# Optimization experiments

Hardware: AMD Instinct MI355X
Metric: run time of the kernel (lower is better)

The kernel has to match this reference:

```python
import jax, jax.numpy as jnp
import numpy as np
import math

DIM = 1024      # dim == dim_attn (required by value-reshape)
HEAD = 16
KV = 128        # K_v routing slots
HD = DIM // HEAD
N = 50000       # number of nodes


def setup_inputs() -> dict:
    key = jax.random.key(0)
    ks = jax.random.split(key, 8)
    s = lambda fan_in: 1.0 / np.sqrt(fan_in)
    return {
        "x": jax.random.normal(ks[0], (N, DIM), jnp.float32),
        "node_index": jax.random.normal(ks[1], (N, 4), jnp.float32),
        # nn.Linear(dim, dim_attn)
        "Wq": jax.random.normal(ks[2], (DIM, DIM), jnp.float32) * s(DIM),
        "bq": jnp.zeros((DIM,), jnp.float32),
        # nn.Parameter key (K_v, head, head_dim), torch.randn init
        "key_p": jax.random.normal(ks[3], (KV, HEAD, HD), jnp.float32),
        # nn.Linear(dim, dim)
        "Wv": jax.random.normal(ks[4], (DIM, DIM), jnp.float32) * s(DIM),
        "bv": jnp.zeros((DIM,), jnp.float32),
        # gate params, shape (head, 1)
        "alpha": jnp.full((HEAD, 1), math.log(9.0), jnp.float32),
        "beta": jnp.full((HEAD, 1), math.log(0.01), jnp.float32),
        # nn.Linear(4, head*K_v)
        "Wb": jax.random.normal(ks[5], (HEAD * KV, 4), jnp.float32) * s(4),
        "bb": jnp.zeros((HEAD * KV,), jnp.float32),
    }


def _mh_sinkhorn(A, num_iters=3, eps=0.05):
    # A: (N, H, K). Faithful to the per-head torch sinkhorn (Q transposed to
    # (K, N)): row sums are over the node axis, col sums over the slot axis.
    n = A.shape[0]
    k = A.shape[2]
    Q = jnp.exp(A / eps)
    Q = Q / jnp.sum(Q, axis=(0, 2), keepdims=True)          # total-sum norm per head
    for _ in range(num_iters):
        Q = Q / jnp.sum(Q, axis=0, keepdims=True) / k       # rows of Q.T (per slot)
        Q = Q / jnp.sum(Q, axis=2, keepdims=True) / n       # cols of Q.T (per node)
    return Q * n


def reference(x, node_index, Wq, bq, key_p, Wv, bv, alpha, beta, Wb, bb):
    n = x.shape[0]
    q = (x @ Wq.T + bq).reshape(n, HEAD, HD)
    attn = jnp.einsum('nhd,rhd->nhr', q, key_p) / np.float32(np.sqrt(HD))
    bias = (node_index @ Wb.T + bb).reshape(n, HEAD, KV)
    attn = attn + bias                                       # (n, H, K_v)
    xv = (x @ Wv.T + bv).reshape(n, HEAD, HD)
    v = jnp.einsum('nhr,nhd->rhd', jax.nn.sigmoid(attn), xv)  # (K_v, H, D)
    cons = _mh_sinkhorn(jax.nn.softmax(attn, axis=-1))
    v = jnp.einsum('nhr,rhd->nhd', cons, v)
    out = jax.nn.sigmoid(alpha) * xv + jax.nn.sigmoid(beta) * v  # (H,1) broadcasts
    return out.reshape(n, DIM)
```

## Files before the change

kernel.cpp:

```cpp
#include <hip/hip_runtime.h>

#define N_NODES 50000
#define MPAD    50176
#define DIM     1024
#define HEAD    16
#define KV      128
#define HD      64
#define NGRP    98

typedef unsigned short ushort_t;
typedef short short8 __attribute__((ext_vector_type(8)));
typedef float f32x4 __attribute__((ext_vector_type(4)));

__device__ inline unsigned short f2bf(float f){
  union { float f; unsigned u; } v; v.f = f;
  unsigned u = v.u;
  unsigned r = (u + 0x7FFFu + ((u >> 16) & 1u)) >> 16;
  return (unsigned short)r;
}
__device__ inline float bf2f(unsigned short u){
  union { unsigned u; float f; } v; v.u = ((unsigned)u) << 16; return v.f;
}

__device__ inline void gload_lds16(const void* g, void* l){
  __builtin_amdgcn_global_load_lds(
      (const __attribute__((address_space(1))) void*)g,
      (__attribute__((address_space(3))) void*)l, 16, 0, 0);
}

__device__ inline short8 frag64(const ushort_t* lds, int row, int kk, int lane){
  int c  = kk*4 + (lane >> 4);
  int cc = c ^ (row & 7);
  return *(const short8*)(lds + row*64 + cc*8);
}
__device__ inline short8 frag128(const ushort_t* lds, int row, int kk, int lane){
  int c  = kk*4 + (lane >> 4);
  int cc = c ^ (row & 7);
  return *(const short8*)(lds + row*128 + cc*8);
}
__device__ inline short8 frag32(const ushort_t* lds, int row, int lane){
  int p = (lane >> 4) ^ ((row >> 1) & 3);
  return *(const short8*)(lds + row*32 + p*8);
}

__global__ void k_zero(float* p, int n){
  int i = blockIdx.x*256 + threadIdx.x;
  if (i < n) p[i] = 0.f;
}

__global__ void k_prep_x(const float* __restrict__ x, ushort_t* __restrict__ x_bf){
  int idx = blockIdx.x*256 + threadIdx.x;
  int row = idx >> 7, c = idx & 127;
  const float4* s = (const float4*)(x + (size_t)row*1024 + c*8);
  float4 f0 = s[0], f1 = s[1];
  short8 v;
  v[0]=(short)f2bf(f0.x); v[1]=(short)f2bf(f0.y); v[2]=(short)f2bf(f0.z); v[3]=(short)f2bf(f0.w);
  v[4]=(short)f2bf(f1.x); v[5]=(short)f2bf(f1.y); v[6]=(short)f2bf(f1.z); v[7]=(short)f2bf(f1.w);
  int sc = (c & ~3) | ((c ^ (row >> 1)) & 3);
  *(short8*)(x_bf + (size_t)row*1024 + sc*8) = v;
}

__global__ void k_prep_w(const float* __restrict__ Wq, const float* __restrict__ Wv,
                         ushort_t* __restrict__ w_bf){
  int idx = blockIdx.x*256 + threadIdx.x;
  int j = idx >> 10, k = idx & 1023;
  float v = (j < 1024) ? Wq[idx] : Wv[(size_t)(j-1024)*1024 + k];
  int l = k >> 3;
  int q = (l & ~3) | ((l ^ (j >> 1)) & 3);
  w_bf[(size_t)j*1024 + q*8 + (k & 7)] = f2bf(v);
}

__global__ void k_prep_key(const float* __restrict__ key_p, ushort_t* __restrict__ key_bf){
  int idx = blockIdx.x*256 + threadIdx.x;
  int h = idx >> 13, rem = idx & 8191;
  int r = rem >> 6, d = rem & 63;
  float v = key_p[(size_t)(r*HEAD + h)*HD + d];
  int pos = ((((d>>3) ^ (r & 7)) & 7) << 3) | (d & 7);
  key_bf[(size_t)h*8192 + r*64 + pos] = f2bf(v);
}

__global__ void k_vreduce(const float* __restrict__ vp, float* __restrict__ vout){
  int i = blockIdx.x*256 + threadIdx.x;
  float s = 0.f;
  for (int gg = 0; gg < NGRP; ++gg) s += vp[(size_t)gg*131072 + i];
  vout[i] = s;
}

__global__ __launch_bounds__(512) void k_gemm(const ushort_t* __restrict__ x_bf,
    const ushort_t* __restrict__ w_bf, const float* __restrict__ bq,
    const float* __restrict__ bv, ushort_t* __restrict__ q_bf, float* xv_out){
  extern __shared__ char gsm[];
  ushort_t* As = (ushort_t*)gsm;
  ushort_t* Bs = (ushort_t*)(gsm + 65536);
  const int tid = threadIdx.x, lane = tid & 63;
  const int wid = tid >> 6, wr = wid >> 2, wc = wid & 3;
  int b = blockIdx.x;
  int wg = (b & 7)*196 + (b >> 3);
  const int bm0 = (wg >> 3) * 256, bn0 = (wg & 7) * 256;

  f32x4 acc[8][4];
  #pragma unroll
  for (int m=0;m<8;m++)
    #pragma unroll
    for (int n=0;n<4;n++) acc[m][n] = (f32x4){0.f,0.f,0.f,0.f};

  const ushort_t* asrc = x_bf + (size_t)bm0*1024;
  const ushort_t* bsrc = w_bf + (size_t)bn0*1024;

#define STAGE(kt, si)                                                     \
  { _Pragma("unroll")                                                     \
    for (int it=0; it<2; ++it){                                           \
      int chunk = it*512 + tid;                                           \
      int r = chunk >> 2, c = chunk & 3;                                  \
      gload_lds16(asrc + (size_t)r*1024 + (kt)*32 + c*8,                  \
                  As + (si)*8192 + chunk*8);                              \
      gload_lds16(bsrc + (size_t)r*1024 + (kt)*32 + c*8,                  \
                  Bs + (si)*8192 + chunk*8);                              \
    }                                                                     \
  }

  STAGE(0, 0);
  STAGE(1, 1);
  STAGE(2, 2);

  for (int t = 0; t < 32; ++t){
    const int cur = t & 3;
    if (t < 30)      { asm volatile("s_waitcnt vmcnt(8)" ::: "memory"); }
    else if (t < 31) { asm volatile("s_waitcnt vmcnt(4)" ::: "memory"); }
    else             { asm volatile("s_waitcnt vmcnt(0)" ::: "memory"); }
    __builtin_amdgcn_s_barrier();
    __builtin_amdgcn_sched_barrier(0);
    if (t + 3 < 32) STAGE(t+3, (t+3)&3);

    const ushort_t* ab  = As + cur*8192;
    const ushort_t* bb_ = Bs + cur*8192;
    short8 bfr[4];
    #pragma unroll
    for (int n=0;n<4;n++) bfr[n] = frag32(bb_, wc*64 + n*16 + (lane&15), lane);
    #pragma unroll
    for (int m=0;m<8;m++){
      short8 af = frag32(ab, wr*128 + m*16 + (lane&15), lane);
      #pragma unroll
      for (int n=0;n<4;n++)
        acc[m][n] = __builtin_amdgcn_mfma_f32_16x16x32_bf16(af, bfr[n], acc[m][n], 0,0,0);
    }
    __builtin_amdgcn_s_barrier();
  }
#undef STAGE

  __syncthreads();

  const bool isq = bn0 < 1024;
  float biasv[4];
  #pragma unroll
  for (int n=0;n<4;n++){
    int col = bn0 + wc*64 + n*16 + (lane & 15);
    biasv[n] = isq ? bq[col] : bv[col - 1024];
  }

  if (isq){
    ushort_t* img = (ushort_t*)gsm;
    #pragma unroll
    for (int n=0;n<4;n++){
      int lcol = wc*64 + n*16 + (lane & 15);
      int d = lcol & 63;
      #pragma unroll
      for (int m=0;m<8;m++){
        #pragma unroll
        for (int j=0;j<4;j++){
          int lrow = wr*128 + m*16 + (lane>>4)*4 + j;
          int sc = (lcol & ~63) | ((((d>>3) ^ (lrow & 7)) & 7) << 3) | (d & 7);
          img[lrow*256 + sc] = f2bf(acc[m][n][j] + biasv[n]);
        }
      }
    }
    __syncthreads();
    #pragma unroll
    for (int it=0; it<16; ++it){
      int r  = it*16 + (tid >> 5);
      int ch = tid & 31;
      short8 v = *(const short8*)(img + r*256 + ch*8);
      *(short8*)(q_bf + (size_t)(bm0 + r)*1024 + bn0 + ch*8) = v;
    }
  } else {
    #pragma unroll
    for (int n=0;n<4;n++){
      int col = bn0 + wc*64 + n*16 + (lane & 15);
      #pragma unroll
      for (int m=0;m<8;m++){
        #pragma unroll
        for (int j=0;j<4;j++){
          int row = bm0 + wr*128 + m*16 + (lane>>4)*4 + j;
          if (row < N_NODES)
            xv_out[(size_t)row*1024 + (col - 1024)] = acc[m][n][j] + biasv[n];
        }
      }
    }
  }
}

template<int PHASE>
__global__ __launch_bounds__(256) void k_attn(
    const ushort_t* __restrict__ q_bf, const ushort_t* __restrict__ key_bf,
    const float* __restrict__ node_index, const float* __restrict__ Wb,
    const float* __restrict__ bb, const float* __restrict__ colsum_in,
    float* __restrict__ colsum_out, const float* __restrict__ v_fin,
    float* __restrict__ v_part, float* xv_out,
    const float* __restrict__ alpha, const float* __restrict__ beta)
{
  constexpr int QB    = (PHASE == 2) ? 1 : 2;
  constexpr int O_Q   = 0;
  constexpr int O_KEY = O_Q + QB*8192;
  constexpr int O_NI  = O_KEY + 16384;
  constexpr int O_WB  = O_NI + QB*1024;
  constexpr int O_RED = O_WB + 2560;
  constexpr int O_COL = O_RED + 2048;
  constexpr int O_W   = O_COL + 512;
  constexpr int O_X1  = O_W + 512;
  constexpr int O_X2  = O_X1 + 16384;

  extern __shared__ char smem[];
  ushort_t* q_lds   = (ushort_t*)(smem + O_Q);
  ushort_t* key_lds = (ushort_t*)(smem + O_KEY);
  float* ni_lds  = (float*)(smem + O_NI);
  float* wb_lds  = (float*)(smem + O_WB);
  float* red_lds = (float*)(smem + O_RED);
  float* col_acc = (float*)(smem + O_COL);
  float* w_lds   = (float*)(smem + O_W);
  ushort_t* sigT     = (ushort_t*)(smem + O_X1);
  ushort_t* xvT      = (ushort_t*)(smem + O_X2);
  ushort_t* vT       = (ushort_t*)(smem + O_X1);
  ushort_t* cons_lds = (ushort_t*)(smem + O_X2);
  float*    out_lds  = (float*)(smem + O_X2);

  const int tid = threadIdx.x, lane = tid & 63, wid = tid >> 6;
  const int h    = blockIdx.x & 15;
  const int g    = blockIdx.x >> 4;
  const int base = g * 512;
  int NT = (MPAD - base) >> 6; if (NT > 8) NT = 8;

  #pragma unroll
  for (int it = 0; it < 4; ++it){
    int chunk = it*256 + tid;
    gload_lds16(key_bf + (size_t)h*8192 + chunk*8, key_lds + chunk*8);
  }
  #pragma unroll
  for (int it = 0; it < 2; ++it){
    int chunk = it*256 + tid;
    int r = chunk >> 3, c = chunk & 7;
    gload_lds16(q_bf + (size_t)(base + r)*1024 + h*64 + c*8, q_lds + chunk*8);
  }
  { int r = tid >> 2, c = tid & 3;
    ni_lds[tid] = (base + r < N_NODES) ? node_index[(size_t)(base + r)*4 + c] : 0.f; }
  if (tid < 128){
    #pragma unroll
    for (int c=0;c<4;c++) wb_lds[tid*5+c] = Wb[(size_t)(h*128 + tid)*4 + c];
    wb_lds[tid*5+4] = bb[h*128 + tid];
    if (PHASE >= 1) w_lds[tid] = 1.f / (128.f * colsum_in[h*128 + tid]);
    if (PHASE <= 1) col_acc[tid] = 0.f;
  }
  if constexpr (PHASE == 2){
    int r = tid >> 1, dh = (tid & 1)*32;
    #pragma unroll
    for (int i=0;i<32;i++){
      int d = dh + i;
      vT[d*128 + ((r>>3) ^ (d&7))*8 + (r&7)] = f2bf(v_fin[((size_t)r*16 + h)*64 + d]);
    }
  }
  float xvr[16], xvn[16];
  if constexpr (PHASE == 0){
    int d = tid & 63, q4 = tid >> 6;
    #pragma unroll
    for (int i=0;i<16;i++){
      int row = base + q4*16 + i;
      xvr[i] = (row < N_NODES) ? xv_out[(size_t)row*1024 + h*64 + d] : 0.f;
    }
  }
  f32x4 vac[2][4];
  if constexpr (PHASE == 0)
    for (int m=0;m<2;m++) for (int n=0;n<4;n++) vac[m][n] = (f32x4){0.f,0.f,0.f,0.f};

  __syncthreads();

  for (int t = 0; t < NT; ++t){
    const int i0  = base + t*64;
    const int cur = t & 1;
    const ushort_t* qb  = q_lds  + ((QB==2) ? cur*4096 : 0);
    const float*    nib = ni_lds + ((QB==2) ? cur*256  : 0);
    float ni_next = 0.f;

    if constexpr (QB == 2){
      if (t+1 < NT){
        int i1 = i0 + 64;
        #pragma unroll
        for (int it = 0; it < 2; ++it){
          int chunk = it*256 + tid;
          int r = chunk >> 3, c = chunk & 7;
          gload_lds16(q_bf + (size_t)(i1 + r)*1024 + h*64 + c*8,
                      q_lds + (cur^1)*4096 + chunk*8);
        }
        int r = tid >> 2, c = tid & 3;
        ni_next = (i0 + 64 + r < N_NODES) ? node_index[(size_t)(i0+64+r)*4 + c] : 0.f;
      }
    } else {
      if (t+1 < NT){
        int r = tid >> 2, c = tid & 3;
        ni_next = (i0 + 64 + r < N_NODES) ? node_index[(size_t)(i0+64+r)*4 + c] : 0.f;
      }
    }
    if constexpr (PHASE == 0){
      if (t+1 < NT){
        int d = tid & 63, q4 = tid >> 6;
        #pragma unroll
        for (int i=0;i<16;i++){
          int row = i0 + 64 + q4*16 + i;
          xvn[i] = (row < N_NODES) ? xv_out[(size_t)row*1024 + h*64 + d] : 0.f;
        }
      }
    }

    f32x4 acc[2][4];
    for (int m=0;m<2;m++) for (int n=0;n<4;n++) acc[m][n] = (f32x4){0.f,0.f,0.f,0.f};
    #pragma unroll
    for (int kk = 0; kk < 2; ++kk){
      short8 kf[2];
      #pragma unroll
      for (int m=0;m<2;m++) kf[m] = frag64(key_lds, wid*32 + m*16 + (lane&15), kk, lane);
      #pragma unroll
      for (int n=0;n<4;n++){
        short8 qf = frag64(qb, n*16 + (lane&15), kk, lane);
        #pragma unroll
        for (int m=0;m<2;m++)
          acc[m][n] = __builtin_amdgcn_mfma_f32_16x16x32_bf16(kf[m], qf, acc[m][n], 0,0,0);
      }
    }

    float nif[4][4];
    #pragma unroll
    for (int n=0;n<4;n++){
      int nn = n*16 + (lane&15);
      #pragma unroll
      for (int c=0;c<4;c++) nif[n][c] = nib[nn*4+c];
    }
    float a[2][4][4];
    #pragma unroll
    for (int m=0;m<2;m++){
      #pragma unroll
      for (int j=0;j<4;j++){
        int r = wid*32 + m*16 + (lane>>4)*4 + j;
        float w0 = wb_lds[r*5+0], w1 = wb_lds[r*5+1];
        float w2 = wb_lds[r*5+2], w3 = wb_lds[r*5+3], w4 = wb_lds[r*5+4];
        #pragma unroll
        for (int n=0;n<4;n++){
          float b = w4 + w0*nif[n][0] + w1*nif[n][1] + w2*nif[n][2] + w3*nif[n][3];
          a[m][n][j] = acc[m][n][j]*0.125f + b;
        }
      }
    }

    float vmask[4];
    #pragma unroll
    for (int n=0;n<4;n++) vmask[n] = (i0 + n*16 + (lane&15) < N_NODES) ? 1.f : 0.f;

    if constexpr (PHASE == 0){
      #pragma unroll
      for (int m=0;m<2;m++) for (int n=0;n<4;n++) for (int j=0;j<4;j++){
        int r  = wid*32 + m*16 + (lane>>4)*4 + j;
        int nn = n*16 + (lane&15);
        float sg = vmask[n] / (1.f + __expf(-a[m][n][j]));
        sigT[r*64 + ((((nn>>3) ^ (r&7)) & 7) << 3) + (nn&7)] = f2bf(sg);
      }
      { int d = tid & 63, q4 = tid >> 6;
        #pragma unroll
        for (int i=0;i<16;i++){
          int nn = q4*16 + i;
          xvT[d*64 + ((((nn>>3) ^ (d&7)) & 7) << 3) + (nn&7)] = f2bf(xvr[i]);
        }
      }
    }

    float pm[4];
    #pragma unroll
    for (int n=0;n<4;n++){
      float m0 = a[0][n][0];
      #pragma unroll
      for (int m=0;m<2;m++) for (int j=0;j<4;j++) m0 = fmaxf(m0, a[m][n][j]);
      m0 = fmaxf(m0, __shfl_xor(m0, 16));
      m0 = fmaxf(m0, __shfl_xor(m0, 32));
      pm[n] = m0;
    }
    if (lane < 16){
      #pragma unroll
      for (int n=0;n<4;n++) red_lds[wid*64 + n*16 + lane] = pm[n];
    }
    __syncthreads();

    if constexpr (QB == 1){
      if (t+1 < NT){
        int i1 = i0 + 64;
        #pragma unroll
        for (int it = 0; it < 2; ++it){
          int chunk = it*256 + tid;
          int r = chunk >> 3, c = chunk & 7;
          gload_lds16(q_bf + (size_t)(i1 + r)*1024 + h*64 + c*8, q_lds + chunk*8);
        }
        ni_lds[tid] = ni_next;
      }
    }

    float mnn[4], snn[4];
    #pragma unroll
    for (int n=0;n<4;n++){
      int nn = n*16 + (lane&15);
      float m0 = red_lds[nn];
      m0 = fmaxf(m0, red_lds[64+nn]); m0 = fmaxf(m0, red_lds[128+nn]); m0 = fmaxf(m0, red_lds[192+nn]);
      mnn[n] = m0;
    }
    #pragma unroll
    for (int n=0;n<4;n++){
      float s = 0.f;
      #pragma unroll
      for (int m=0;m<2;m++) for (int j=0;j<4;j++){
        float e = __expf(a[m][n][j] - mnn[n]);
        a[m][n][j] = e; s += e;
      }
      s += __shfl_xor(s, 16); s += __shfl_xor(s, 32);
      snn[n] = s;
    }
    if (lane < 16){
      #pragma unroll
      for (int n=0;n<4;n++) red_lds[256 + wid*64 + n*16 + lane] = snn[n];
    }

    if constexpr (PHASE == 0){
      #pragma unroll
      for (int kk=0;kk<2;kk++){
        short8 sa[2];
        #pragma unroll
        for (int m=0;m<2;m++) sa[m] = frag64(sigT, wid*32 + m*16 + (lane&15), kk, lane);
        #pragma unroll
        for (int n=0;n<4;n++){
          short8 xf = frag64(xvT, n*16 + (lane&15), kk, lane);
          #pragma unroll
          for (int m=0;m<2;m++)
            vac[m][n] = __builtin_amdgcn_mfma_f32_16x16x32_bf16(sa[m], xf, vac[m][n], 0,0,0);
        }
      }
    }
    __syncthreads();

    #pragma unroll
    for (int n=0;n<4;n++){
      int nn = n*16 + (lane&15);
      snn[n] = red_lds[256+nn] + red_lds[256+64+nn] + red_lds[256+128+nn] + red_lds[256+192+nn];
    }
    #pragma unroll
    for (int n=0;n<4;n++){
      float inv = 20.f / snn[n];
      #pragma unroll
      for (int m=0;m<2;m++) for (int j=0;j<4;j++)
        a[m][n][j] = __expf(a[m][n][j] * inv);
    }

    float uval[4];
    if constexpr (PHASE >= 1){
      #pragma unroll
      for (int n=0;n<4;n++){
        float s = 0.f;
        #pragma unroll
        for (int m=0;m<2;m++){
          #pragma unroll
          for (int j=0;j<4;j++){
            int r = wid*32 + m*16 + (lane>>4)*4 + j;
            s += a[m][n][j] * w_lds[r];
          }
        }
        s += __shfl_xor(s, 16); s += __shfl_xor(s, 32);
        uval[n] = s;
      }
      if (lane < 16){
        #pragma unroll
        for (int n=0;n<4;n++) red_lds[wid*64 + n*16 + lane] = uval[n];
      }
      __syncthreads();
      #pragma unroll
      for (int n=0;n<4;n++){
        int nn = n*16 + (lane&15);
        float s = red_lds[nn] + red_lds[64+nn] + red_lds[128+nn] + red_lds[192+nn];
        uval[n] = 1.f / (50000.f * s);
      }
    }

    if constexpr (PHASE <= 1){
      float cs[2][4];
      #pragma unroll
      for (int m=0;m<2;m++){
        #pragma unroll
        for (int j=0;j<4;j++){
          float s = 0.f;
          #pragma unroll
          for (int n=0;n<4;n++){
            float tv = a[m][n][j] * vmask[n];
            if (PHASE == 1) tv *= uval[n];
            s += tv;
          }
          s += __shfl_xor(s, 1); s += __shfl_xor(s, 2);
          s += __shfl_xor(s, 4); s += __shfl_xor(s, 8);
          cs[m][j] = s;
        }
      }
      if ((lane & 15) == 0){
        #pragma unroll
        for (int m=0;m<2;m++) for (int j=0;j<4;j++){
          int r = wid*32 + m*16 + (lane>>4)*4 + j;
          col_acc[r] += cs[m][j];
        }
      }
    }

    if constexpr (PHASE == 2){
      #pragma unroll
      for (int m=0;m<2;m++) for (int n=0;n<4;n++) for (int j=0;j<4;j++){
        int r  = wid*32 + m*16 + (lane>>4)*4 + j;
        int nn = n*16 + (lane&15);
        float cv = 50000.f * uval[n] * a[m][n][j] * w_lds[r];
        cons_lds[nn*128 + ((r>>3) ^ (nn&7))*8 + (r&7)] = f2bf(cv);
      }
      __syncthreads();
      f32x4 oac[4];
      for (int n=0;n<4;n++) oac[n] = (f32x4){0.f,0.f,0.f,0.f};
      #pragma unroll
      for (int kk=0;kk<4;kk++){
        short8 va = frag128(vT, wid*16 + (lane&15), kk, lane);
        #pragma unroll
        for (int n=0;n<4;n++){
          short8 cf = frag128(cons_lds, n*16 + (lane&15), kk, lane);
          oac[n] = __builtin_amdgcn_mfma_f32_16x16x32_bf16(va, cf, oac[n], 0,0,0);
        }
      }
      __syncthreads();
      #pragma unroll
      for (int n=0;n<4;n++) for (int j=0;j<4;j++){
        int d  = wid*16 + (lane>>4)*4 + j;
        int nn = n*16 + (lane&15);
        out_lds[nn*68 + d] = oac[n][j];
      }
      __syncthreads();
      float sa = 1.f/(1.f + __expf(-alpha[h]));
      float sb = 1.f/(1.f + __expf(-beta[h]));
      int nn = tid >> 2, d0 = (tid & 3)*16;
      if (i0 + nn < N_NODES){
        #pragma unroll
        for (int gq=0; gq<4; ++gq){
          float4 vf = *(const float4*)(out_lds + nn*68 + d0 + gq*4);
          float4 xf = *(const float4*)(xv_out + (size_t)(i0+nn)*1024 + h*64 + d0 + gq*4);
          float4 o;
          o.x = sa*xf.x + sb*vf.x;
          o.y = sa*xf.y + sb*vf.y;
          o.z = sa*xf.z + sb*vf.z;
          o.w = sa*xf.w + sb*vf.w;
          *(float4*)(xv_out + (size_t)(i0+nn)*1024 + h*64 + d0 + gq*4) = o;
        }
      }
    } else {
      if (t+1 < NT && QB == 2) ni_lds[(cur^1)*256 + tid] = ni_next;
      if constexpr (PHASE == 0){
        if (t+1 < NT){
          #pragma unroll
          for (int i=0;i<16;i++) xvr[i] = xvn[i];
        }
      }
      __syncthreads();
    }
  }

  if constexpr (PHASE == 0){
    float* vdst = v_part + (size_t)g*131072;
    #pragma unroll
    for (int m=0;m<2;m++) for (int n=0;n<4;n++) for (int j=0;j<4;j++){
      int r = wid*32 + m*16 + (lane>>4)*4 + j;
      int d = n*16 + (lane&15);
      vdst[((size_t)r*16 + h)*64 + d] = vac[m][n][j];
    }
  }
  if constexpr (PHASE <= 1){
    if (tid < 128) atomicAdd(&colsum_out[h*128 + tid], col_acc[tid]);
  }
}

extern "C" void kernel_launch(void* const* d_in, const int* in_sizes, int n_in,
                              void* d_out, int out_size, void* d_ws, size_t ws_size,
                              hipStream_t stream){
  const float* x     = (const float*)d_in[0];
  const float* ni    = (const float*)d_in[1];
  const float* Wq    = (const float*)d_in[2];
  const float* bq    = (const float*)d_in[3];
  const float* keyp  = (const float*)d_in[4];
  const float* Wv    = (const float*)d_in[5];
  const float* bv    = (const float*)d_in[6];
  const float* alpha = (const float*)d_in[7];
  const float* beta  = (const float*)d_in[8];
  const float* Wb    = (const float*)d_in[9];
  const float* bb    = (const float*)d_in[10];
  float* out = (float*)d_out;

  char* ws = (char*)d_ws;
  ushort_t* x_bf   = (ushort_t*)(ws);
  float*    v_part = (float*)(ws);
  ushort_t* q_bf   = (ushort_t*)(ws + 102760448);
  ushort_t* w_bf   = (ushort_t*)(ws + 205520896);
  ushort_t* key_bf = (ushort_t*)(ws + 209715200);
  float*    v_fin  = (float*)(ws + 209977344);
  float*    cs     = (float*)(ws + 210501632);

  (void)hipFuncSetAttribute((const void*)k_gemm,
      hipFuncAttributeMaxDynamicSharedMemorySize, 131072);

  k_zero<<<dim3(24), 256, 0, stream>>>(cs, 6144);
  k_zero<<<dim3(352), 256, 0, stream>>>((float*)(x_bf + (size_t)N_NODES*1024), 90112);
  k_prep_x<<<dim3(25000), 256, 0, stream>>>(x, x_bf);
  k_prep_w<<<dim3(2048*1024/256), 256, 0, stream>>>(Wq, Wv, w_bf);
  k_prep_key<<<dim3(HEAD*KV*HD/256), 256, 0, stream>>>(keyp, key_bf);
  k_gemm<<<dim3(1568), 512, 131072, stream>>>(x_bf, w_bf, bq, bv, q_bf, out);

  dim3 ag(NGRP*16);
  k_attn<0><<<ag, 256, 65024, stream>>>(q_bf, key_bf, ni, Wb, bb, nullptr,  cs,      v_fin, v_part, out, alpha, beta);
  k_vreduce<<<dim3(512), 256, 0, stream>>>(v_part, v_fin);
  k_attn<1><<<ag, 256, 40448, stream>>>(q_bf, key_bf, ni, Wb, bb, cs,       cs+2048, v_fin, v_part, out, alpha, beta);
  k_attn<1><<<ag, 256, 40448, stream>>>(q_bf, key_bf, ni, Wb, bb, cs+2048,  cs+4096, v_fin, v_part, out, alpha, beta);
  k_attn<2><<<ag, 256, 65024, stream>>>(q_bf, key_bf, ni, Wb, bb, cs+4096,  nullptr, v_fin, v_part, out, alpha, beta);
}
```

Measured before the change: 952.7 us.

## Restructure QV GEMM main loop into ping-pong double-buffered half-tile schedule

Replaces the 4-stage single-K-slice LDS ring in the fused Q/V projection GEMM with two 64-wide K buffers, each split into two 32-wide subtiles. Each subtile is consumed in two M-halves, with explicit barriers interleaving LDS fragment reads, global-to-LDS prefetches and MFMA bursts. MFMA sections run at raised wave priority via s_setprio. The aim is better overlap of LDS reads and global loads with matrix math and fewer idle MFMA cycles. In exchange it adds more barriers per K step and depends on fragile manual vmcnt accounting.

```diff
diff --git a/kernel.cpp b/kernel.cpp
--- a/kernel.cpp
+++ b/kernel.cpp
@@ -37,10 +37,6 @@
   int c  = kk*4 + (lane >> 4);
   int cc = c ^ (row & 7);
   return *(const short8*)(lds + row*128 + cc*8);
-}
-__device__ inline short8 frag32(const ushort_t* lds, int row, int lane){
-  int p = (lane >> 4) ^ ((row >> 1) & 3);
-  return *(const short8*)(lds + row*32 + p*8);
 }
 
 __global__ void k_zero(float* p, int n){
@@ -90,13 +86,13 @@
     const ushort_t* __restrict__ w_bf, const float* __restrict__ bq,
     const float* __restrict__ bv, ushort_t* __restrict__ q_bf, float* xv_out){
   extern __shared__ char gsm[];
-  ushort_t* As = (ushort_t*)gsm;
-  ushort_t* Bs = (ushort_t*)(gsm + 65536);
+  ushort_t* lds = (ushort_t*)gsm;
   const int tid = threadIdx.x, lane = tid & 63;
   const int wid = tid >> 6, wr = wid >> 2, wc = wid & 3;
   int b = blockIdx.x;
   int wg = (b & 7)*196 + (b >> 3);
   const int bm0 = (wg >> 3) * 256, bn0 = (wg & 7) * 256;
+  const int pA = (lane >> 4) ^ ((lane >> 1) & 3);
 
   f32x4 acc[8][4];
   #pragma unroll
@@ -107,46 +103,81 @@
   const ushort_t* asrc = x_bf + (size_t)bm0*1024;
   const ushort_t* bsrc = w_bf + (size_t)bn0*1024;
 
-#define STAGE(kt, si)                                                     \
-  { _Pragma("unroll")                                                     \
+#define STG(kt, kk, bi) do{                                               \
+    _Pragma("unroll")                                                     \
     for (int it=0; it<2; ++it){                                           \
-      int chunk = it*512 + tid;                                           \
-      int r = chunk >> 2, c = chunk & 3;                                  \
-      gload_lds16(asrc + (size_t)r*1024 + (kt)*32 + c*8,                  \
-                  As + (si)*8192 + chunk*8);                              \
-      gload_lds16(bsrc + (size_t)r*1024 + (kt)*32 + c*8,                  \
-                  Bs + (si)*8192 + chunk*8);                              \
-    }                                                                     \
-  }
-
-  STAGE(0, 0);
-  STAGE(1, 1);
-  STAGE(2, 2);
-
-  for (int t = 0; t < 32; ++t){
-    const int cur = t & 3;
-    if (t < 30)      { asm volatile("s_waitcnt vmcnt(8)" ::: "memory"); }
-    else if (t < 31) { asm volatile("s_waitcnt vmcnt(4)" ::: "memory"); }
-    else             { asm volatile("s_waitcnt vmcnt(0)" ::: "memory"); }
-    __builtin_amdgcn_s_barrier();
-    __builtin_amdgcn_sched_barrier(0);
-    if (t + 3 < 32) STAGE(t+3, (t+3)&3);
-
-    const ushort_t* ab  = As + cur*8192;
-    const ushort_t* bb_ = Bs + cur*8192;
-    short8 bfr[4];
-    #pragma unroll
-    for (int n=0;n<4;n++) bfr[n] = frag32(bb_, wc*64 + n*16 + (lane&15), lane);
-    #pragma unroll
-    for (int m=0;m<8;m++){
-      short8 af = frag32(ab, wr*128 + m*16 + (lane&15), lane);
-      #pragma unroll
-      for (int n=0;n<4;n++)
-        acc[m][n] = __builtin_amdgcn_mfma_f32_16x16x32_bf16(af, bfr[n], acc[m][n], 0,0,0);
-    }
-    __builtin_amdgcn_s_barrier();
-  }
-#undef STAGE
+      int ch = it*512 + tid; int r = ch>>2, c = ch&3;                     \
+      gload_lds16(asrc + (size_t)r*1024 + (kt)*64 + (kk)*32 + c*8,        \
+                  lds + (bi)*32768 + (kk)*8192 + ch*8);                   \
+      gload_lds16(bsrc + (size_t)r*1024 + (kt)*64 + (kk)*32 + c*8,        \
+                  lds + (bi)*32768 + 16384 + (kk)*8192 + ch*8);           \
+    } }while(0)
+
+#define RD_A(BASE, KK, MH)                                                \
+    _Pragma("unroll")                                                     \
+    for (int m=0;m<4;m++){                                                \
+      int row = wr*128 + ((MH)*4+m)*16 + (lane&15);                       \
+      af[m] = *(const short8*)((BASE) + (KK)*8192 + row*32 + pA*8);       \
+    }
+#define RD_B(BASE, KK)                                                    \
+    _Pragma("unroll")                                                     \
+    for (int n=0;n<4;n++){                                                \
+      int row = wc*64 + n*16 + (lane&15);                                 \
+      bf_[n] = *(const short8*)((BASE) + 16384 + (KK)*8192 + row*32 + pA*8); \
+    }
+#define MFMA16(MH)                                                        \
+    __builtin_amdgcn_s_setprio(1);                                        \
+    _Pragma("unroll")                                                     \
+    for (int m=0;m<4;m++)                                                 \
+      _Pragma("unroll")                                                   \
+      for (int n=0;n<4;n++)                                               \
+        acc[(MH)*4+m][n] = __builtin_amdgcn_mfma_f32_16x16x32_bf16(       \
+            af[m], bf_[n], acc[(MH)*4+m][n], 0,0,0);                      \
+    __builtin_amdgcn_s_setprio(0);
+#define BAR asm volatile("s_barrier" ::: "memory")
+
+  STG(0,0,0); STG(0,1,0); STG(1,0,1);
+  asm volatile("s_waitcnt vmcnt(8)" ::: "memory");
+  BAR;
+
+  for (int t = 0; t < 16; ++t){
+    const int bufc = t & 1, bufn = bufc ^ 1;
+    const ushort_t* base = lds + bufc*32768;
+    short8 af[4], bf_[4];
+
+    RD_B(base, 0);
+    RD_A(base, 0, 0);
+    if (t+1 < 16) STG(t+1, 1, bufn);
+    BAR;
+    MFMA16(0);
+    BAR;
+
+    RD_A(base, 0, 1);
+    BAR;
+    MFMA16(1);
+    if (t == 15) { asm volatile("s_waitcnt vmcnt(0)" ::: "memory"); }
+    else         { asm volatile("s_waitcnt vmcnt(8)" ::: "memory"); }
+    BAR;
+
+    RD_B(base, 1);
+    RD_A(base, 1, 0);
+    if (t+2 < 16) STG(t+2, 0, bufc);
+    BAR;
+    MFMA16(0);
+    BAR;
+
+    RD_A(base, 1, 1);
+    BAR;
+    MFMA16(1);
+    if (t <= 13)      { asm volatile("s_waitcnt vmcnt(8)" ::: "memory"); }
+    else if (t == 14) { asm volatile("s_waitcnt vmcnt(4)" ::: "memory"); }
+    BAR;
+  }
+#undef STG
+#undef RD_A
+#undef RD_B
+#undef MFMA16
+#undef BAR
 
   __syncthreads();
 
```

Result: no change. 951.0 us (-0.2%).
